# Performance work log

Measured on AMD Instinct MI355X. Metric: run time of the kernel, lower is better.

Reference implementation:

```python
import jax, jax.numpy as jnp
import numpy as np

N = 50000   # nodes
E = 640000  # edges
G = 128     # graphs in batch
H = 128     # hidden_channels
F_NODE, F_EDGE, F_LIG, F_POC = 64, 16, 200, 100
N_STACK = 3  # num_layers - 1


def setup_inputs() -> dict:
    key = jax.random.key(0)
    ks = jax.random.split(key, 24)
    r = lambda i, shape, s=0.05: jax.random.normal(ks[i], shape, dtype=jnp.float32) * s
    z = lambda shape: jnp.zeros(shape, jnp.float32)
    return {
        "x": jax.random.normal(ks[0], (N, F_NODE), dtype=jnp.float32),
        "edge_index": jax.random.randint(ks[1], (2, E), 0, N),
        "edge_attr": jax.random.normal(ks[2], (E, F_EDGE), dtype=jnp.float32),
        "batch": jnp.sort(jax.random.randint(ks[3], (N,), 0, G)),
        "ligand_features": jax.random.normal(ks[4], (G, F_LIG), dtype=jnp.float32),
        "pocket_features": jax.random.normal(ks[5], (G, F_POC), dtype=jnp.float32),
        # conv1 (in != out -> lin_self is a Linear)
        "W1_msg": r(6, (F_NODE, H)), "b1_msg": z((H,)),
        "W1_edge": r(7, (F_EDGE, H)), "b1_edge": z((H,)),
        "W1_self": r(8, (F_NODE, H)), "b1_self": z((H,)),
        # stacked convs (in == out -> lin_self is Identity)
        "Wk_msg": r(9, (N_STACK, H, H)), "bk_msg": z((N_STACK, H)),
        "Wk_edge": r(10, (N_STACK, F_EDGE, H)), "bk_edge": z((N_STACK, H)),
        # global feature / fusion / output heads
        "Wl": r(11, (F_LIG, H)), "bl": z((H,)),
        "Wp": r(12, (F_POC, H)), "bp": z((H,)),
        "Wf": r(13, (3 * H, H)), "bf": z((H,)),
        "Wo": r(14, (H, 1)), "bo": z((1,)),
        "return_embeddings": 0,
    }


def _general_conv(x, edge_index, edge_attr, W_msg, b_msg, W_edge, b_edge, self_out):
    # PyG GeneralConv: msg = lin_msg(x_src) + lin_edge(edge_attr), sum-aggregated at dst,
    # then + lin_self(x) (Identity skip when passed self_out = x).
    src, dst = edge_index[0], edge_index[1]
    edge_term = edge_attr @ W_edge + b_edge            # [E, H] (per-edge, layer-specific)
    msg = x[src] @ W_msg + b_msg + edge_term           # [E, H] gather + GEMM
    agg = jax.ops.segment_sum(msg, dst, num_segments=x.shape[0])  # scatter-add
    return agg + self_out


def reference(x, edge_index, edge_attr, batch, ligand_features, pocket_features,
              W1_msg, b1_msg, W1_edge, b1_edge, W1_self, b1_self,
              Wk_msg, bk_msg, Wk_edge, bk_edge,
              Wl, bl, Wp, bp, Wf, bf, Wo, bo, return_embeddings):
    # conv1 with linear self-connection
    h = _general_conv(x, edge_index, edge_attr, W1_msg, b1_msg, W1_edge, b1_edge,
                      x @ W1_self + b1_self)
    h = jax.nn.relu(h)
    # stacked convs with identity self-connection
    for i in range(N_STACK):
        h = _general_conv(h, edge_index, edge_attr, Wk_msg[i], bk_msg[i],
                          Wk_edge[i], bk_edge[i], h)
        h = jax.nn.relu(h)
    # global mean pool over graphs
    sums = jax.ops.segment_sum(h, batch, num_segments=G)
    counts = jax.ops.segment_sum(jnp.ones((h.shape[0],), h.dtype), batch, num_segments=G)
    pooled = sums / jnp.maximum(counts, 1.0)[:, None]
    # global feature fusion
    lig = ligand_features @ Wl + bl
    poc = pocket_features @ Wp + bp
    fused = jnp.concatenate([pooled, lig, poc], axis=1) @ Wf + bf
    # dropout is a no-op in eval mode
    if not return_embeddings:
        fused = fused @ Wo + bo
    return fused
```

## Files before the change

### kernel.cpp

```cpp
#include <hip/hip_runtime.h>
#include <cstdint>

#define NN 50000
#define NE 640000
#define NG 128
#define HD 128
#define FN 64
#define FE 16
#define FL 200
#define FPOC 100
#define NSTACK 3

typedef unsigned short ushort_t;
typedef short short8 __attribute__((ext_vector_type(8)));
typedef float f32x4 __attribute__((ext_vector_type(4)));

__device__ __forceinline__ ushort_t f2bf(float f) {
    unsigned u = __float_as_uint(f);
    unsigned r = (u + 0x7fffu + ((u >> 16) & 1u)) >> 16;
    return (ushort_t)r;
}
__device__ __forceinline__ float bf2f(ushort_t u) {
    return __uint_as_float(((unsigned)u) << 16);
}


__global__ void count_kernel(const int* __restrict__ ei, int* __restrict__ cnt) {
    int e = blockIdx.x * 256 + threadIdx.x;
    if (e < NE) atomicAdd(&cnt[ei[NE + e]], 1);
}

__global__ void bsum_kernel(const int* __restrict__ cnt, int* __restrict__ bsum) {
    __shared__ int s[256];
    int t = threadIdx.x;
    int i = blockIdx.x * 256 + t;
    int v = (i < NN) ? cnt[i] : 0;
    s[t] = v;
    __syncthreads();
    for (int off = 128; off > 0; off >>= 1) {
        if (t < off) s[t] += s[t + off];
        __syncthreads();
    }
    if (t == 0) bsum[blockIdx.x] = s[0];
}

__global__ void bscan_kernel(const int* __restrict__ bsum, int* __restrict__ bpre, int nb) {
    __shared__ int s[256];
    int t = threadIdx.x;
    int v = (t < nb) ? bsum[t] : 0;
    s[t] = v;
    __syncthreads();
    for (int off = 1; off < 256; off <<= 1) {
        int w = (t >= off) ? s[t - off] : 0;
        __syncthreads();
        s[t] += w;
        __syncthreads();
    }
    if (t < nb) bpre[t] = s[t] - v;
}

__global__ void rowptr_kernel(const int* __restrict__ cnt, const int* __restrict__ bpre,
                              int* __restrict__ row_ptr) {
    __shared__ int s[256];
    int t = threadIdx.x;
    int i = blockIdx.x * 256 + t;
    int v = (i < NN) ? cnt[i] : 0;
    s[t] = v;
    __syncthreads();
    for (int off = 1; off < 256; off <<= 1) {
        int w = (t >= off) ? s[t - off] : 0;
        __syncthreads();
        s[t] += w;
        __syncthreads();
    }
    if (i < NN) row_ptr[i] = s[t] - v + bpre[blockIdx.x];
    if (i == 0) row_ptr[NN] = NE;
}

__global__ void fill_kernel(const int* __restrict__ ei, const int* __restrict__ row_ptr,
                            int* __restrict__ cnt, int2* __restrict__ csr) {
    int e = blockIdx.x * 256 + threadIdx.x;
    if (e < NE) {
        int s = ei[e];
        int d = ei[NE + e];
        int old = atomicSub(&cnt[d], 1);
        csr[row_ptr[d] + old - 1] = make_int2(s, e);
    }
}

__global__ __launch_bounds__(256) void sege_kernel(
    const int* __restrict__ row_ptr, const int2* __restrict__ csr,
    const float* __restrict__ ea, ushort_t* __restrict__ segaug) {
    int node = blockIdx.x * 4 + (threadIdx.x >> 6);
    if (node >= NN) return;
    int lane = threadIdx.x & 63;
    int G = lane >> 2, q4 = (lane & 3) * 4;
    int beg = row_ptr[node], end = row_ptr[node + 1];
    float4 a = make_float4(0.f, 0.f, 0.f, 0.f);
    for (int j = beg + G; j < end; j += 16) {
        int e = csr[j].y;
        float4 v = *(const float4*)(ea + (size_t)e * FE + q4);
        a.x += v.x; a.y += v.y; a.z += v.z; a.w += v.w;
    }
    for (int m = 4; m <= 32; m <<= 1) {
        a.x += __shfl_xor(a.x, m);
        a.y += __shfl_xor(a.y, m);
        a.z += __shfl_xor(a.z, m);
        a.w += __shfl_xor(a.w, m);
    }
    if (lane < 4) {
        ushort_t o[4] = {f2bf(a.x), f2bf(a.y), f2bf(a.z), f2bf(a.w)};
        *(uint2*)(segaug + (size_t)node * 32 + lane * 4) = *(uint2*)o;
    } else if (lane < 8) {
        ushort_t o[4] = {0, 0, 0, 0};
        if (lane == 4) { o[0] = f2bf((float)(end - beg)); o[1] = f2bf(1.f); }
        *(uint2*)(segaug + (size_t)node * 32 + lane * 4) = *(uint2*)o;
    }
}


__global__ void repack_kernel(const float* __restrict__ W1_msg,
                              const float* __restrict__ W1_self,
                              const float* __restrict__ W1_edge,
                              const float* __restrict__ b1_msg,
                              const float* __restrict__ b1_edge,
                              const float* __restrict__ b1_self,
                              const float* __restrict__ Wk_msg,
                              const float* __restrict__ Wk_edge,
                              const float* __restrict__ bk_msg,
                              const float* __restrict__ bk_edge,
                              ushort_t* __restrict__ pack) {
    int mid = blockIdx.y;
    const float *W = nullptr, *bm = nullptr, *be = nullptr, *bc = nullptr;
    int K;
    size_t doff;
    bool aug = false;
    if (mid == 0)      { W = W1_msg;  K = 64;  doff = 0; }
    else if (mid == 1) { W = W1_self; K = 64;  doff = 8192; }
    else if (mid == 2) { W = W1_edge; bm = b1_msg; be = b1_edge; bc = b1_self;
                         K = 32; doff = 16384; aug = true; }
    else if (mid <= 5) { int i = mid - 3; W = Wk_msg + (size_t)i * HD * HD;
                         K = 128; doff = 20480 + (size_t)i * 16384; }
    else               { int i = mid - 6; W = Wk_edge + (size_t)i * FE * HD;
                         bm = bk_msg + i * HD; be = bk_edge + i * HD;
                         K = 32; doff = 69632 + (size_t)i * 4096; aug = true; }
    int KS = K / 32;
    int t = blockIdx.x * 256 + threadIdx.x;
    if (t >= 8 * KS * 64) return;
    int lane = t & 63;
    int nk = t >> 6;
    int ks = nk % KS, nt = nk / KS;
    int n = nt * 16 + (lane & 15);
    int kb = ks * 32 + (lane >> 4) * 8;
    ushort_t o[8];
#pragma unroll
    for (int j = 0; j < 8; ++j) {
        int k = kb + j;
        float v;
        if (!aug)         v = W[(size_t)k * HD + n];
        else if (k < 16)  v = W[(size_t)k * HD + n];
        else if (k == 16) v = bm[n] + be[n];
        else if (k == 17) v = bc ? bc[n] : 0.f;
        else              v = 0.f;
        o[j] = f2bf(v);
    }
    *(uint4*)(pack + doff + (size_t)t * 8) = *(uint4*)o;
}


__global__ __launch_bounds__(256) void gemm_mfma_conv1(const float* __restrict__ A,
                                                       const ushort_t* __restrict__ segaug,
                                                       const ushort_t* __restrict__ pack,
                                                       ushort_t* __restrict__ Cm,
                                                       ushort_t* __restrict__ Cs, int n) {
    constexpr int STR = 72, SSTR = 40;
    __shared__ __align__(16) ushort_t As[64 * STR];
    __shared__ __align__(16) ushort_t Ss[64 * SSTR];
    int tid = threadIdx.x;
    int row0 = blockIdx.x * 64;
#pragma unroll
    for (int p = 0; p < 2; ++p) {
        int c = p * 256 + tid;
        int r = c >> 3, col = (c & 7) * 8;
        int gr = row0 + r;
        float4 f0 = make_float4(0.f, 0.f, 0.f, 0.f), f1 = f0;
        if (gr < n) {
            f0 = *(const float4*)(A + (size_t)gr * FN + col);
            f1 = *(const float4*)(A + (size_t)gr * FN + col + 4);
        }
        ushort_t o[8] = {f2bf(f0.x), f2bf(f0.y), f2bf(f0.z), f2bf(f0.w),
                         f2bf(f1.x), f2bf(f1.y), f2bf(f1.z), f2bf(f1.w)};
        *(uint4*)(&As[r * STR + col]) = *(uint4*)o;
    }
    {
        int c = tid;
        int r = c >> 2, col = (c & 3) * 8;
        int gr = row0 + r;
        uint4 v = make_uint4(0u, 0u, 0u, 0u);
        if (gr < n) v = *(const uint4*)(segaug + (size_t)gr * 32 + col);
        *(uint4*)(&Ss[r * SSTR + col]) = v;
    }
    __syncthreads();
    int lane = tid & 63, wave = tid >> 6;
    int m = lane & 15, quad = lane >> 4;
    f32x4 acc[16];
#pragma unroll
    for (int i = 0; i < 16; ++i) acc[i] = (f32x4)(0.f);
    const short8* Bmsg = (const short8*)pack;
    const short8* Bself = (const short8*)(pack + 8192);
    const short8* Beaug = (const short8*)(pack + 16384);
#pragma unroll
    for (int ks = 0; ks < 2; ++ks) {
        short8 a = *(const short8*)(&As[(wave * 16 + m) * STR + ks * 32 + quad * 8]);
#pragma unroll
        for (int nt = 0; nt < 8; ++nt) {
            acc[nt] = __builtin_amdgcn_mfma_f32_16x16x32_bf16(
                a, Bmsg[(nt * 2 + ks) * 64 + lane], acc[nt], 0, 0, 0);
            acc[8 + nt] = __builtin_amdgcn_mfma_f32_16x16x32_bf16(
                a, Bself[(nt * 2 + ks) * 64 + lane], acc[8 + nt], 0, 0, 0);
        }
    }
    {
        short8 sa = *(const short8*)(&Ss[(wave * 16 + m) * SSTR + quad * 8]);
#pragma unroll
        for (int nt = 0; nt < 8; ++nt)
            acc[8 + nt] = __builtin_amdgcn_mfma_f32_16x16x32_bf16(
                sa, Beaug[nt * 64 + lane], acc[8 + nt], 0, 0, 0);
    }
#pragma unroll
    for (int nt = 0; nt < 8; ++nt) {
        int col = nt * 16 + m;
#pragma unroll
        for (int r = 0; r < 4; ++r) {
            int grow = row0 + wave * 16 + quad * 4 + r;
            if (grow < n) {
                Cm[(size_t)grow * HD + col] = f2bf(acc[nt][r]);
                Cs[(size_t)grow * HD + col] = f2bf(acc[8 + nt][r]);
            }
        }
    }
}


__device__ __forceinline__ void accum8(float* a, uint4 v) {
    a[0] += __uint_as_float(v.x << 16);
    a[1] += __uint_as_float(v.x & 0xffff0000u);
    a[2] += __uint_as_float(v.y << 16);
    a[3] += __uint_as_float(v.y & 0xffff0000u);
    a[4] += __uint_as_float(v.z << 16);
    a[5] += __uint_as_float(v.z & 0xffff0000u);
    a[6] += __uint_as_float(v.w << 16);
    a[7] += __uint_as_float(v.w & 0xffff0000u);
}

__global__ __launch_bounds__(256, 6) void fused_agg_gemm(
    const int* __restrict__ row_ptr, const int2* __restrict__ csr,
    const ushort_t* __restrict__ msg_in, const ushort_t* __restrict__ S_in,
    const ushort_t* __restrict__ segaug, const ushort_t* __restrict__ Bm,
    const ushort_t* __restrict__ Be, ushort_t* __restrict__ msg_out,
    ushort_t* __restrict__ S_out) {
    constexpr int STR = 136, SSTR = 40;
    __shared__ __align__(16) ushort_t Hs[16 * STR];
    __shared__ __align__(16) ushort_t Ss[16 * SSTR];
    int tid = threadIdx.x;
    int node0 = blockIdx.x * 16;
    if (tid < 64) {
        int r = tid >> 2, col = (tid & 3) * 8;
        *(uint4*)(&Ss[r * SSTR + col]) =
            *(const uint4*)(segaug + (size_t)(node0 + r) * 32 + col);
    }
    int nl = tid >> 4;
    int node = node0 + nl;
    int c8 = (tid & 15) * 8;
    int beg = row_ptr[node], end = row_ptr[node + 1];
    float a0[8] = {0.f, 0.f, 0.f, 0.f, 0.f, 0.f, 0.f, 0.f};
    float a1[8] = {0.f, 0.f, 0.f, 0.f, 0.f, 0.f, 0.f, 0.f};
    int j = beg;
    for (; j + 3 < end; j += 4) {
        int u0 = csr[j].x, u1 = csr[j + 1].x, u2 = csr[j + 2].x, u3 = csr[j + 3].x;
        uint4 v0 = *(const uint4*)(msg_in + (size_t)u0 * HD + c8);
        uint4 v1 = *(const uint4*)(msg_in + (size_t)u1 * HD + c8);
        uint4 v2 = *(const uint4*)(msg_in + (size_t)u2 * HD + c8);
        uint4 v3 = *(const uint4*)(msg_in + (size_t)u3 * HD + c8);
        accum8(a0, v0);
        accum8(a1, v1);
        accum8(a0, v2);
        accum8(a1, v3);
    }
    for (; j < end; ++j) {
        uint4 v = *(const uint4*)(msg_in + (size_t)csr[j].x * HD + c8);
        accum8(a0, v);
    }
    accum8(a0, *(const uint4*)(S_in + (size_t)node * HD + c8));
    {
        ushort_t h8[8];
#pragma unroll
        for (int i = 0; i < 8; ++i) h8[i] = f2bf(fmaxf(a0[i] + a1[i], 0.f));
        *(uint4*)(&Hs[nl * STR + c8]) = *(uint4*)h8;
    }
    __syncthreads();
    int lane = tid & 63, wave = tid >> 6;
    int m = lane & 15, quad = lane >> 4;
    f32x4 acc[2], accE[2];
#pragma unroll
    for (int t = 0; t < 2; ++t) { acc[t] = (f32x4)(0.f); accE[t] = (f32x4)(0.f); }
    const short8* Bmv = (const short8*)Bm;
    const short8* Bev = (const short8*)Be;
#pragma unroll
    for (int ks = 0; ks < 4; ++ks) {
        short8 a = *(const short8*)(&Hs[m * STR + ks * 32 + quad * 8]);
#pragma unroll
        for (int t = 0; t < 2; ++t) {
            int nt = wave * 2 + t;
            acc[t] = __builtin_amdgcn_mfma_f32_16x16x32_bf16(
                a, Bmv[(nt * 4 + ks) * 64 + lane], acc[t], 0, 0, 0);
        }
    }
    {
        short8 sa = *(const short8*)(&Ss[m * SSTR + quad * 8]);
#pragma unroll
        for (int t = 0; t < 2; ++t) {
            int nt = wave * 2 + t;
            accE[t] = __builtin_amdgcn_mfma_f32_16x16x32_bf16(
                sa, Bev[nt * 64 + lane], accE[t], 0, 0, 0);
        }
    }
#pragma unroll
    for (int t = 0; t < 2; ++t) {
        int col = (wave * 2 + t) * 16 + m;
#pragma unroll
        for (int r = 0; r < 4; ++r) {
            int rl = quad * 4 + r;
            size_t gidx = (size_t)(node0 + rl) * HD + col;
            msg_out[gidx] = f2bf(acc[t][r]);
            S_out[gidx] = f2bf(accE[t][r] + bf2f(Hs[rl * STR + col]));
        }
    }
}


__global__ __launch_bounds__(256, 6) void agg_pool_kernel(
    const int* __restrict__ row_ptr, const int2* __restrict__ csr,
    const ushort_t* __restrict__ xm, const ushort_t* __restrict__ selfb,
    const int* __restrict__ batch, float* __restrict__ pooled) {
    __shared__ float hloc[16][HD];
    int tid = threadIdx.x;
    int node0 = blockIdx.x * 16;
    int nl = tid >> 4;
    int node = node0 + nl;
    int c8 = (tid & 15) * 8;
    int beg = row_ptr[node], end = row_ptr[node + 1];
    float a0[8] = {0.f, 0.f, 0.f, 0.f, 0.f, 0.f, 0.f, 0.f};
    float a1[8] = {0.f, 0.f, 0.f, 0.f, 0.f, 0.f, 0.f, 0.f};
    int j = beg;
    for (; j + 3 < end; j += 4) {
        int u0 = csr[j].x, u1 = csr[j + 1].x, u2 = csr[j + 2].x, u3 = csr[j + 3].x;
        uint4 v0 = *(const uint4*)(xm + (size_t)u0 * HD + c8);
        uint4 v1 = *(const uint4*)(xm + (size_t)u1 * HD + c8);
        uint4 v2 = *(const uint4*)(xm + (size_t)u2 * HD + c8);
        uint4 v3 = *(const uint4*)(xm + (size_t)u3 * HD + c8);
        accum8(a0, v0);
        accum8(a1, v1);
        accum8(a0, v2);
        accum8(a1, v3);
    }
    for (; j < end; ++j) {
        uint4 v = *(const uint4*)(xm + (size_t)csr[j].x * HD + c8);
        accum8(a0, v);
    }
    accum8(a0, *(const uint4*)(selfb + (size_t)node * HD + c8));
#pragma unroll
    for (int i = 0; i < 8; ++i) hloc[nl][c8 + i] = fmaxf(a0[i] + a1[i], 0.f);
    __syncthreads();
    if (tid < HD) {
        int f = tid;
        float run = 0.f;
        int gprev = batch[node0];
        for (int r = 0; r < 16; ++r) {
            int g = batch[node0 + r];
            if (g != gprev) {
                atomicAdd(&pooled[gprev * HD + f], run);
                run = 0.f;
                gprev = g;
            }
            run += hloc[r][f];
        }
        atomicAdd(&pooled[gprev * HD + f], run);
    }
}


__global__ void head_kernel(const float* __restrict__ pooled, const int* __restrict__ batch,
                            const float* __restrict__ lf, const float* __restrict__ pfe,
                            const float* __restrict__ Wl, const float* __restrict__ bl,
                            const float* __restrict__ Wp, const float* __restrict__ bp,
                            const float* __restrict__ Wf, const float* __restrict__ bfv,
                            const float* __restrict__ Wo, const float* __restrict__ bo,
                            float* __restrict__ out) {
    __shared__ float cat[3 * HD];
    __shared__ float red[HD];
    int g = blockIdx.x, j = threadIdx.x;
    int lo = 0, hi = NN;
    while (lo < hi) { int m = (lo + hi) >> 1; if (batch[m] < g) lo = m + 1; else hi = m; }
    int s0 = lo;
    lo = s0; hi = NN;
    while (lo < hi) { int m = (lo + hi) >> 1; if (batch[m] < g + 1) lo = m + 1; else hi = m; }
    float cntf = (float)(lo - s0);
    cat[j] = pooled[(size_t)g * HD + j] / fmaxf(cntf, 1.f);
    float s = bl[j];
    for (int k = 0; k < FL; ++k) s += lf[g * FL + k] * Wl[k * HD + j];
    cat[HD + j] = s;
    s = bp[j];
    for (int k = 0; k < FPOC; ++k) s += pfe[g * FPOC + k] * Wp[k * HD + j];
    cat[2 * HD + j] = s;
    __syncthreads();
    float fj = bfv[j];
    for (int k = 0; k < 3 * HD; ++k) fj += cat[k] * Wf[k * HD + j];
    red[j] = fj * Wo[j];
    __syncthreads();
    for (int off = 64; off > 0; off >>= 1) {
        if (j < off) red[j] += red[j + off];
        __syncthreads();
    }
    if (j == 0) out[g] = red[0] + bo[0];
}


extern "C" void kernel_launch(void* const* d_in, const int* in_sizes, int n_in,
                              void* d_out, int out_size, void* d_ws, size_t ws_size,
                              hipStream_t stream) {
    const float* x       = (const float*)d_in[0];
    const int*   ei      = (const int*)d_in[1];
    const float* ea      = (const float*)d_in[2];
    const int*   batch   = (const int*)d_in[3];
    const float* lf      = (const float*)d_in[4];
    const float* pfe     = (const float*)d_in[5];
    const float* W1_msg  = (const float*)d_in[6];
    const float* b1_msg  = (const float*)d_in[7];
    const float* W1_edge = (const float*)d_in[8];
    const float* b1_edge = (const float*)d_in[9];
    const float* W1_self = (const float*)d_in[10];
    const float* b1_self = (const float*)d_in[11];
    const float* Wk_msg  = (const float*)d_in[12];
    const float* bk_msg  = (const float*)d_in[13];
    const float* Wk_edge = (const float*)d_in[14];
    const float* bk_edge = (const float*)d_in[15];
    const float* Wl      = (const float*)d_in[16];
    const float* bl      = (const float*)d_in[17];
    const float* Wp      = (const float*)d_in[18];
    const float* bp      = (const float*)d_in[19];
    const float* Wf      = (const float*)d_in[20];
    const float* bfv     = (const float*)d_in[21];
    const float* Wo      = (const float*)d_in[22];
    const float* bo      = (const float*)d_in[23];

    char* wsp = (char*)d_ws;
    size_t off = 0;
    auto carve = [&](size_t bytes) -> void* {
        char* p = wsp + off;
        off += (bytes + 255) & ~(size_t)255;
        return (void*)p;
    };
    int*      cnt     = (int*)carve((size_t)NN * 4);
    float*    pooled  = (float*)carve((size_t)NG * HD * 4);
    int*      row_ptr = (int*)carve((size_t)(NN + 1) * 4);
    int2*     csr     = (int2*)carve((size_t)NE * 8);
    ushort_t* segaug  = (ushort_t*)carve((size_t)NN * 32 * 2);
    ushort_t* pack    = (ushort_t*)carve((size_t)81920 * 2);
    ushort_t* bufC    = (ushort_t*)carve((size_t)NN * HD * 2);
    ushort_t* bufD    = (ushort_t*)carve((size_t)NN * HD * 2);
    ushort_t* bufS    = (ushort_t*)carve((size_t)NN * HD * 2);
    ushort_t* bufT    = (ushort_t*)carve((size_t)NN * HD * 2);
    int*      bsum    = (int*)carve((size_t)256 * 4);
    int*      bpre    = (int*)carve((size_t)256 * 4);

    const int NBLK = (NN + 255) / 256;

    size_t clr = (size_t)((char*)(pooled + NG * HD) - (char*)cnt);
    hipMemsetAsync(cnt, 0, clr, stream);

    count_kernel<<<(NE + 255) / 256, 256, 0, stream>>>(ei, cnt);
    bsum_kernel<<<NBLK, 256, 0, stream>>>(cnt, bsum);
    bscan_kernel<<<1, 256, 0, stream>>>(bsum, bpre, NBLK);
    rowptr_kernel<<<NBLK, 256, 0, stream>>>(cnt, bpre, row_ptr);
    fill_kernel<<<(NE + 255) / 256, 256, 0, stream>>>(ei, row_ptr, cnt, csr);
    sege_kernel<<<(NN + 3) / 4, 256, 0, stream>>>(row_ptr, csr, ea, segaug);
    repack_kernel<<<dim3(8, 9), 256, 0, stream>>>(W1_msg, W1_self, W1_edge, b1_msg,
                                                  b1_edge, b1_self, Wk_msg, Wk_edge,
                                                  bk_msg, bk_edge, pack);

    gemm_mfma_conv1<<<dim3((NN + 63) / 64), 256, 0, stream>>>(x, segaug, pack, bufC,
                                                              bufS, NN);
    fused_agg_gemm<<<NN / 16, 256, 0, stream>>>(row_ptr, csr, bufC, bufS, segaug,
                                                pack + 20480, pack + 69632, bufD, bufT);
    fused_agg_gemm<<<NN / 16, 256, 0, stream>>>(row_ptr, csr, bufD, bufT, segaug,
                                                pack + 20480 + 16384, pack + 69632 + 4096,
                                                bufC, bufS);
    fused_agg_gemm<<<NN / 16, 256, 0, stream>>>(row_ptr, csr, bufC, bufS, segaug,
                                                pack + 20480 + 32768, pack + 69632 + 8192,
                                                bufD, bufT);
    agg_pool_kernel<<<NN / 16, 256, 0, stream>>>(row_ptr, csr, bufD, bufT, batch, pooled);

    head_kernel<<<NG, HD, 0, stream>>>(pooled, batch, lf, pfe, Wl, bl, Wp, bp, Wf, bfv,
                                       Wo, bo, (float*)d_out);
}
```

Baseline: 388.3 us.

## Build CSR with atomic block allocation and stage neighbor indices in LDS

The three-kernel prefix scan is replaced by a single alloc kernel. Each 256-node block takes its base offset with one atomicAdd, and fill uses per-node cursors, so row_ptr becomes row_beg plus cnt and two launches go away. The aggregation kernels copy each 16-node tile's source indices into shared memory, unroll the gather loop to 8 loads in flight, and prefetch the self row, aiming for more memory-level parallelism in the irregular gather. Segment order across blocks becomes nondeterministic, and the extra LDS plus the launch-bounds change from 6 to 5 may reduce occupancy.

```diff
diff --git a/kernel.cpp b/kernel.cpp
--- a/kernel.cpp
+++ b/kernel.cpp
@@ -10,6 +10,7 @@
 #define FL 200
 #define FPOC 100
 #define NSTACK 3
+#define EDGE_CAP 512
 
 typedef unsigned short ushort_t;
 typedef short short8 __attribute__((ext_vector_type(8)));
@@ -30,24 +31,13 @@
     if (e < NE) atomicAdd(&cnt[ei[NE + e]], 1);
 }
 
-__global__ void bsum_kernel(const int* __restrict__ cnt, int* __restrict__ bsum) {
+__global__ void alloc_kernel(const int* __restrict__ cnt, int* __restrict__ row_beg,
+                             int* __restrict__ cur, int* __restrict__ gtot) {
     __shared__ int s[256];
+    __shared__ int base;
     int t = threadIdx.x;
     int i = blockIdx.x * 256 + t;
     int v = (i < NN) ? cnt[i] : 0;
-    s[t] = v;
-    __syncthreads();
-    for (int off = 128; off > 0; off >>= 1) {
-        if (t < off) s[t] += s[t + off];
-        __syncthreads();
-    }
-    if (t == 0) bsum[blockIdx.x] = s[0];
-}
-
-__global__ void bscan_kernel(const int* __restrict__ bsum, int* __restrict__ bpre, int nb) {
-    __shared__ int s[256];
-    int t = threadIdx.x;
-    int v = (t < nb) ? bsum[t] : 0;
     s[t] = v;
     __syncthreads();
     for (int off = 1; off < 256; off <<= 1) {
@@ -56,46 +46,37 @@
         s[t] += w;
         __syncthreads();
     }
-    if (t < nb) bpre[t] = s[t] - v;
-}
-
-__global__ void rowptr_kernel(const int* __restrict__ cnt, const int* __restrict__ bpre,
-                              int* __restrict__ row_ptr) {
-    __shared__ int s[256];
-    int t = threadIdx.x;
-    int i = blockIdx.x * 256 + t;
-    int v = (i < NN) ? cnt[i] : 0;
-    s[t] = v;
-    __syncthreads();
-    for (int off = 1; off < 256; off <<= 1) {
-        int w = (t >= off) ? s[t - off] : 0;
-        __syncthreads();
-        s[t] += w;
-        __syncthreads();
-    }
-    if (i < NN) row_ptr[i] = s[t] - v + bpre[blockIdx.x];
-    if (i == 0) row_ptr[NN] = NE;
-}
-
-__global__ void fill_kernel(const int* __restrict__ ei, const int* __restrict__ row_ptr,
-                            int* __restrict__ cnt, int2* __restrict__ csr) {
+    if (t == 255) base = atomicAdd(gtot, s[255]);
+    __syncthreads();
+    if (i < NN) {
+        int b = base + s[t] - v;
+        row_beg[i] = b;
+        cur[i] = b;
+    }
+}
+
+__global__ void fill_kernel(const int* __restrict__ ei, int* __restrict__ cur,
+                            int2* __restrict__ csr) {
     int e = blockIdx.x * 256 + threadIdx.x;
     if (e < NE) {
         int s = ei[e];
         int d = ei[NE + e];
-        int old = atomicSub(&cnt[d], 1);
-        csr[row_ptr[d] + old - 1] = make_int2(s, e);
+        int pos = atomicAdd(&cur[d], 1);
+        csr[pos] = make_int2(s, e);
     }
 }
 
 __global__ __launch_bounds__(256) void sege_kernel(
-    const int* __restrict__ row_ptr, const int2* __restrict__ csr,
-    const float* __restrict__ ea, ushort_t* __restrict__ segaug) {
+    const int* __restrict__ row_beg, const int* __restrict__ cnt,
+    const int2* __restrict__ csr, const float* __restrict__ ea,
+    ushort_t* __restrict__ segaug) {
     int node = blockIdx.x * 4 + (threadIdx.x >> 6);
     if (node >= NN) return;
     int lane = threadIdx.x & 63;
     int G = lane >> 2, q4 = (lane & 3) * 4;
-    int beg = row_ptr[node], end = row_ptr[node + 1];
+    int beg = row_beg[node];
+    int dg = cnt[node];
+    int end = beg + dg;
     float4 a = make_float4(0.f, 0.f, 0.f, 0.f);
     for (int j = beg + G; j < end; j += 16) {
         int e = csr[j].y;
@@ -113,7 +94,7 @@
         *(uint2*)(segaug + (size_t)node * 32 + lane * 4) = *(uint2*)o;
     } else if (lane < 8) {
         ushort_t o[4] = {0, 0, 0, 0};
-        if (lane == 4) { o[0] = f2bf((float)(end - beg)); o[1] = f2bf(1.f); }
+        if (lane == 4) { o[0] = f2bf((float)dg); o[1] = f2bf(1.f); }
         *(uint2*)(segaug + (size_t)node * 32 + lane * 4) = *(uint2*)o;
     }
 }
@@ -253,15 +234,47 @@
     a[7] += __uint_as_float(v.w & 0xffff0000u);
 }
 
-__global__ __launch_bounds__(256, 6) void fused_agg_gemm(
-    const int* __restrict__ row_ptr, const int2* __restrict__ csr,
-    const ushort_t* __restrict__ msg_in, const ushort_t* __restrict__ S_in,
-    const ushort_t* __restrict__ segaug, const ushort_t* __restrict__ Bm,
-    const ushort_t* __restrict__ Be, ushort_t* __restrict__ msg_out,
-    ushort_t* __restrict__ S_out) {
+#define GET_LDS(jj) (ce[lb + (jj)])
+#define GET_GBL(jj) (csr[(size_t)(beg + (jj))].x)
+
+#define AGG_BODY(GET)                                                        \
+    {                                                                        \
+        int j = 0;                                                           \
+        for (; j + 7 < d; j += 8) {                                          \
+            int u[8];                                                        \
+            _Pragma("unroll") for (int t = 0; t < 8; ++t) u[t] = GET(j + t); \
+            uint4 v[8];                                                      \
+            _Pragma("unroll") for (int t = 0; t < 8; ++t)                    \
+                v[t] = *(const uint4*)(msg_in + (size_t)u[t] * HD + c8);     \
+            _Pragma("unroll") for (int t = 0; t < 8; ++t)                    \
+                accum8((t & 1) ? a1 : a0, v[t]);                             \
+        }                                                                    \
+        if (j + 3 < d) {                                                     \
+            int u[4];                                                        \
+            _Pragma("unroll") for (int t = 0; t < 4; ++t) u[t] = GET(j + t); \
+            uint4 v[4];                                                      \
+            _Pragma("unroll") for (int t = 0; t < 4; ++t)                    \
+                v[t] = *(const uint4*)(msg_in + (size_t)u[t] * HD + c8);     \
+            _Pragma("unroll") for (int t = 0; t < 4; ++t)                    \
+                accum8((t & 1) ? a1 : a0, v[t]);                             \
+            j += 4;                                                          \
+        }                                                                    \
+        for (; j < d; ++j) {                                                 \
+            uint4 v = *(const uint4*)(msg_in + (size_t)GET(j) * HD + c8);    \
+            accum8(a0, v);                                                   \
+        }                                                                    \
+    }
+
+__global__ __launch_bounds__(256, 5) void fused_agg_gemm(
+    const int* __restrict__ row_beg, const int* __restrict__ cnt,
+    const int2* __restrict__ csr, const ushort_t* __restrict__ msg_in,
+    const ushort_t* __restrict__ S_in, const ushort_t* __restrict__ segaug,
+    const ushort_t* __restrict__ Bm, const ushort_t* __restrict__ Be,
+    ushort_t* __restrict__ msg_out, ushort_t* __restrict__ S_out) {
     constexpr int STR = 136, SSTR = 40;
     __shared__ __align__(16) ushort_t Hs[16 * STR];
     __shared__ __align__(16) ushort_t Ss[16 * SSTR];
+    __shared__ int ce[EDGE_CAP];
     int tid = threadIdx.x;
     int node0 = blockIdx.x * 16;
     if (tid < 64) {
@@ -269,29 +282,26 @@
         *(uint4*)(&Ss[r * SSTR + col]) =
             *(const uint4*)(segaug + (size_t)(node0 + r) * 32 + col);
     }
+    int b0 = row_beg[node0];
+    int nE = row_beg[node0 + 15] + cnt[node0 + 15] - b0;
+    int stg = nE < EDGE_CAP ? nE : EDGE_CAP;
+    for (int i = tid; i < stg; i += 256) ce[i] = csr[b0 + i].x;
     int nl = tid >> 4;
     int node = node0 + nl;
     int c8 = (tid & 15) * 8;
-    int beg = row_ptr[node], end = row_ptr[node + 1];
+    int beg = row_beg[node];
+    int d = cnt[node];
+    int lb = beg - b0;
+    uint4 sv = *(const uint4*)(S_in + (size_t)node * HD + c8);
+    __syncthreads();
     float a0[8] = {0.f, 0.f, 0.f, 0.f, 0.f, 0.f, 0.f, 0.f};
     float a1[8] = {0.f, 0.f, 0.f, 0.f, 0.f, 0.f, 0.f, 0.f};
-    int j = beg;
-    for (; j + 3 < end; j += 4) {
-        int u0 = csr[j].x, u1 = csr[j + 1].x, u2 = csr[j + 2].x, u3 = csr[j + 3].x;
-        uint4 v0 = *(const uint4*)(msg_in + (size_t)u0 * HD + c8);
-        uint4 v1 = *(const uint4*)(msg_in + (size_t)u1 * HD + c8);
-        uint4 v2 = *(const uint4*)(msg_in + (size_t)u2 * HD + c8);
-        uint4 v3 = *(const uint4*)(msg_in + (size_t)u3 * HD + c8);
-        accum8(a0, v0);
-        accum8(a1, v1);
-        accum8(a0, v2);
-        accum8(a1, v3);
-    }
-    for (; j < end; ++j) {
-        uint4 v = *(const uint4*)(msg_in + (size_t)csr[j].x * HD + c8);
-        accum8(a0, v);
-    }
-    accum8(a0, *(const uint4*)(S_in + (size_t)node * HD + c8));
+    if (lb + d <= EDGE_CAP) {
+        AGG_BODY(GET_LDS)
+    } else {
+        AGG_BODY(GET_GBL)
+    }
+    accum8(a0, sv);
     {
         ushort_t h8[8];
 #pragma unroll
@@ -339,36 +349,36 @@
 }
 
 
-__global__ __launch_bounds__(256, 6) void agg_pool_kernel(
-    const int* __restrict__ row_ptr, const int2* __restrict__ csr,
-    const ushort_t* __restrict__ xm, const ushort_t* __restrict__ selfb,
-    const int* __restrict__ batch, float* __restrict__ pooled) {
+__global__ __launch_bounds__(256, 5) void agg_pool_kernel(
+    const int* __restrict__ row_beg, const int* __restrict__ cnt,
+    const int2* __restrict__ csr, const ushort_t* __restrict__ xm,
+    const ushort_t* __restrict__ selfb, const int* __restrict__ batch,
+    float* __restrict__ pooled) {
     __shared__ float hloc[16][HD];
+    __shared__ int ce[EDGE_CAP];
     int tid = threadIdx.x;
     int node0 = blockIdx.x * 16;
+    int b0 = row_beg[node0];
+    int nE = row_beg[node0 + 15] + cnt[node0 + 15] - b0;
+    int stg = nE < EDGE_CAP ? nE : EDGE_CAP;
+    for (int i = tid; i < stg; i += 256) ce[i] = csr[b0 + i].x;
     int nl = tid >> 4;
     int node = node0 + nl;
     int c8 = (tid & 15) * 8;
-    int beg = row_ptr[node], end = row_ptr[node + 1];
+    int beg = row_beg[node];
+    int d = cnt[node];
+    int lb = beg - b0;
+    const ushort_t* msg_in = xm;
+    uint4 sv = *(const uint4*)(selfb + (size_t)node * HD + c8);
+    __syncthreads();
     float a0[8] = {0.f, 0.f, 0.f, 0.f, 0.f, 0.f, 0.f, 0.f};
     float a1[8] = {0.f, 0.f, 0.f, 0.f, 0.f, 0.f, 0.f, 0.f};
-    int j = beg;
-    for (; j + 3 < end; j += 4) {
-        int u0 = csr[j].x, u1 = csr[j + 1].x, u2 = csr[j + 2].x, u3 = csr[j + 3].x;
-        uint4 v0 = *(const uint4*)(xm + (size_t)u0 * HD + c8);
-        uint4 v1 = *(const uint4*)(xm + (size_t)u1 * HD + c8);
-        uint4 v2 = *(const uint4*)(xm + (size_t)u2 * HD + c8);
-        uint4 v3 = *(const uint4*)(xm + (size_t)u3 * HD + c8);
-        accum8(a0, v0);
-        accum8(a1, v1);
-        accum8(a0, v2);
-        accum8(a1, v3);
-    }
-    for (; j < end; ++j) {
-        uint4 v = *(const uint4*)(xm + (size_t)csr[j].x * HD + c8);
-        accum8(a0, v);
-    }
-    accum8(a0, *(const uint4*)(selfb + (size_t)node * HD + c8));
+    if (lb + d <= EDGE_CAP) {
+        AGG_BODY(GET_LDS)
+    } else {
+        AGG_BODY(GET_GBL)
+    }
+    accum8(a0, sv);
 #pragma unroll
     for (int i = 0; i < 8; ++i) hloc[nl][c8 + i] = fmaxf(a0[i] + a1[i], 0.f);
     __syncthreads();
@@ -462,8 +472,10 @@
         return (void*)p;
     };
     int*      cnt     = (int*)carve((size_t)NN * 4);
+    int*      misc    = (int*)carve(256);
     float*    pooled  = (float*)carve((size_t)NG * HD * 4);
-    int*      row_ptr = (int*)carve((size_t)(NN + 1) * 4);
+    int*      row_beg = (int*)carve((size_t)NN * 4);
+    int*      cur     = (int*)carve((size_t)NN * 4);
     int2*     csr     = (int2*)carve((size_t)NE * 8);
     ushort_t* segaug  = (ushort_t*)carve((size_t)NN * 32 * 2);
     ushort_t* pack    = (ushort_t*)carve((size_t)81920 * 2);
@@ -471,8 +483,6 @@
     ushort_t* bufD    = (ushort_t*)carve((size_t)NN * HD * 2);
     ushort_t* bufS    = (ushort_t*)carve((size_t)NN * HD * 2);
     ushort_t* bufT    = (ushort_t*)carve((size_t)NN * HD * 2);
-    int*      bsum    = (int*)carve((size_t)256 * 4);
-    int*      bpre    = (int*)carve((size_t)256 * 4);
 
     const int NBLK = (NN + 255) / 256;
 
@@ -480,26 +490,25 @@
     hipMemsetAsync(cnt, 0, clr, stream);
 
     count_kernel<<<(NE + 255) / 256, 256, 0, stream>>>(ei, cnt);
-    bsum_kernel<<<NBLK, 256, 0, stream>>>(cnt, bsum);
-    bscan_kernel<<<1, 256, 0, stream>>>(bsum, bpre, NBLK);
-    rowptr_kernel<<<NBLK, 256, 0, stream>>>(cnt, bpre, row_ptr);
-    fill_kernel<<<(NE + 255) / 256, 256, 0, stream>>>(ei, row_ptr, cnt, csr);
-    sege_kernel<<<(NN + 3) / 4, 256, 0, stream>>>(row_ptr, csr, ea, segaug);
+    alloc_kernel<<<NBLK, 256, 0, stream>>>(cnt, row_beg, cur, misc);
+    fill_kernel<<<(NE + 255) / 256, 256, 0, stream>>>(ei, cur, csr);
+    sege_kernel<<<(NN + 3) / 4, 256, 0, stream>>>(row_beg, cnt, csr, ea, segaug);
     repack_kernel<<<dim3(8, 9), 256, 0, stream>>>(W1_msg, W1_self, W1_edge, b1_msg,
                                                   b1_edge, b1_self, Wk_msg, Wk_edge,
                                                   bk_msg, bk_edge, pack);
 
     gemm_mfma_conv1<<<dim3((NN + 63) / 64), 256, 0, stream>>>(x, segaug, pack, bufC,
                                                               bufS, NN);
-    fused_agg_gemm<<<NN / 16, 256, 0, stream>>>(row_ptr, csr, bufC, bufS, segaug,
+    fused_agg_gemm<<<NN / 16, 256, 0, stream>>>(row_beg, cnt, csr, bufC, bufS, segaug,
                                                 pack + 20480, pack + 69632, bufD, bufT);
-    fused_agg_gemm<<<NN / 16, 256, 0, stream>>>(row_ptr, csr, bufD, bufT, segaug,
+    fused_agg_gemm<<<NN / 16, 256, 0, stream>>>(row_beg, cnt, csr, bufD, bufT, segaug,
                                                 pack + 20480 + 16384, pack + 69632 + 4096,
                                                 bufC, bufS);
-    fused_agg_gemm<<<NN / 16, 256, 0, stream>>>(row_ptr, csr, bufC, bufS, segaug,
+    fused_agg_gemm<<<NN / 16, 256, 0, stream>>>(row_beg, cnt, csr, bufC, bufS, segaug,
                                                 pack + 20480 + 32768, pack + 69632 + 8192,
                                                 bufD, bufT);
-    agg_pool_kernel<<<NN / 16, 256, 0, stream>>>(row_ptr, csr, bufD, bufT, batch, pooled);
+    agg_pool_kernel<<<NN / 16, 256, 0, stream>>>(row_beg, cnt, csr, bufD, bufT, batch,
+                                                 pooled);
 
     head_kernel<<<NG, HD, 0, stream>>>(pooled, batch, lf, pfe, Wl, bl, Wp, bp, Wf, bfv,
                                        Wo, bo, (float*)d_out);
```

Result: slower. 397.3 us (+2.3%).

## Build CSR via two-level bucket sort with shared-memory atomics

Applied to the files above, without the earlier changes.

Replaces the per-node global-atomic count, three-kernel scan and global-atomic fill with a bucketed counting sort. Edges are first binned into 196 buckets of 256 destination nodes using shared-memory histograms and a staging buffer. A per-bucket kernel then computes node offsets and places edges with shared-memory atomics. Downstream kernels switch from row_ptr to row_beg plus a count. This cuts global atomic contention and kernel launches, at the cost of an extra staging array and a second pass over the edges.

```diff
diff --git a/kernel.cpp b/kernel.cpp
--- a/kernel.cpp
+++ b/kernel.cpp
@@ -10,6 +10,7 @@
 #define FL 200
 #define FPOC 100
 #define NSTACK 3
+#define NBUK 196
 
 typedef unsigned short ushort_t;
 typedef short short8 __attribute__((ext_vector_type(8)));
@@ -25,29 +26,26 @@
 }
 
 
-__global__ void count_kernel(const int* __restrict__ ei, int* __restrict__ cnt) {
-    int e = blockIdx.x * 256 + threadIdx.x;
-    if (e < NE) atomicAdd(&cnt[ei[NE + e]], 1);
-}
-
-__global__ void bsum_kernel(const int* __restrict__ cnt, int* __restrict__ bsum) {
+__global__ void hist_kernel(const int* __restrict__ ei, int* __restrict__ bucket_cnt) {
+    __shared__ int l[NBUK];
+    int t = threadIdx.x;
+    if (t < NBUK) l[t] = 0;
+    __syncthreads();
+    int base = blockIdx.x * 2048;
+#pragma unroll
+    for (int i = 0; i < 8; ++i) {
+        int e = base + i * 256 + t;
+        if (e < NE) atomicAdd(&l[ei[NE + e] >> 8], 1);
+    }
+    __syncthreads();
+    if (t < NBUK && l[t]) atomicAdd(&bucket_cnt[t], l[t]);
+}
+
+__global__ void scan_kernel(const int* __restrict__ bucket_cnt,
+                            int* __restrict__ bucket_base, int* __restrict__ bucket_cur) {
     __shared__ int s[256];
     int t = threadIdx.x;
-    int i = blockIdx.x * 256 + t;
-    int v = (i < NN) ? cnt[i] : 0;
-    s[t] = v;
-    __syncthreads();
-    for (int off = 128; off > 0; off >>= 1) {
-        if (t < off) s[t] += s[t + off];
-        __syncthreads();
-    }
-    if (t == 0) bsum[blockIdx.x] = s[0];
-}
-
-__global__ void bscan_kernel(const int* __restrict__ bsum, int* __restrict__ bpre, int nb) {
-    __shared__ int s[256];
-    int t = threadIdx.x;
-    int v = (t < nb) ? bsum[t] : 0;
+    int v = (t < NBUK) ? bucket_cnt[t] : 0;
     s[t] = v;
     __syncthreads();
     for (int off = 1; off < 256; off <<= 1) {
@@ -56,46 +54,97 @@
         s[t] += w;
         __syncthreads();
     }
-    if (t < nb) bpre[t] = s[t] - v;
-}
-
-__global__ void rowptr_kernel(const int* __restrict__ cnt, const int* __restrict__ bpre,
-                              int* __restrict__ row_ptr) {
-    __shared__ int s[256];
+    if (t < NBUK) {
+        int b = s[t] - v;
+        bucket_base[t] = b;
+        bucket_cur[t] = b;
+    }
+}
+
+__global__ __launch_bounds__(256) void scatter_bin(const int* __restrict__ ei,
+                                                   int* __restrict__ bucket_cur,
+                                                   int2* __restrict__ staging) {
+    __shared__ int lcnt[NBUK];
+    __shared__ int lrun[NBUK];
     int t = threadIdx.x;
-    int i = blockIdx.x * 256 + t;
-    int v = (i < NN) ? cnt[i] : 0;
-    s[t] = v;
+    if (t < NBUK) lcnt[t] = 0;
+    __syncthreads();
+    int base = blockIdx.x * 4096;
+#pragma unroll
+    for (int i = 0; i < 16; ++i) {
+        int e = base + i * 256 + t;
+        if (e < NE) atomicAdd(&lcnt[ei[NE + e] >> 8], 1);
+    }
+    __syncthreads();
+    if (t < NBUK) {
+        int c = lcnt[t];
+        lrun[t] = c ? atomicAdd(&bucket_cur[t], c) : 0;
+        lcnt[t] = 0;
+    }
+    __syncthreads();
+#pragma unroll
+    for (int i = 0; i < 16; ++i) {
+        int e = base + i * 256 + t;
+        if (e < NE) {
+            int s = ei[e];
+            int d = ei[NE + e];
+            int bk = d >> 8;
+            int off = atomicAdd(&lcnt[bk], 1);
+            staging[lrun[bk] + off] = make_int2(s, e | ((d & 255) << 20));
+        }
+    }
+}
+
+__global__ __launch_bounds__(256) void place_kernel(
+    const int* __restrict__ bucket_base, const int* __restrict__ bucket_cnt,
+    const int2* __restrict__ staging, int* __restrict__ row_beg,
+    int* __restrict__ cnt, int2* __restrict__ csr) {
+    __shared__ int hist[256];
+    __shared__ int curp[256];
+    int t = threadIdx.x;
+    int b = blockIdx.x;
+    int n0 = b << 8;
+    hist[t] = 0;
+    __syncthreads();
+    int ebase = bucket_base[b];
+    int ecnt = bucket_cnt[b];
+    for (int i = t; i < ecnt; i += 256) atomicAdd(&hist[staging[ebase + i].y >> 20], 1);
+    __syncthreads();
+    int v = hist[t];
     __syncthreads();
     for (int off = 1; off < 256; off <<= 1) {
-        int w = (t >= off) ? s[t - off] : 0;
+        int w = (t >= off) ? hist[t - off] : 0;
         __syncthreads();
-        s[t] += w;
+        hist[t] += w;
         __syncthreads();
     }
-    if (i < NN) row_ptr[i] = s[t] - v + bpre[blockIdx.x];
-    if (i == 0) row_ptr[NN] = NE;
-}
-
-__global__ void fill_kernel(const int* __restrict__ ei, const int* __restrict__ row_ptr,
-                            int* __restrict__ cnt, int2* __restrict__ csr) {
-    int e = blockIdx.x * 256 + threadIdx.x;
-    if (e < NE) {
-        int s = ei[e];
-        int d = ei[NE + e];
-        int old = atomicSub(&cnt[d], 1);
-        csr[row_ptr[d] + old - 1] = make_int2(s, e);
+    int rb = ebase + hist[t] - v;
+    if (n0 + t < NN) {
+        row_beg[n0 + t] = rb;
+        cnt[n0 + t] = v;
+    }
+    curp[t] = rb;
+    __syncthreads();
+    for (int i = t; i < ecnt; i += 256) {
+        int2 p = staging[ebase + i];
+        int dl = p.y >> 20;
+        int e = p.y & 0xFFFFF;
+        int pos = atomicAdd(&curp[dl], 1);
+        csr[pos] = make_int2(p.x, e);
     }
 }
 
 __global__ __launch_bounds__(256) void sege_kernel(
-    const int* __restrict__ row_ptr, const int2* __restrict__ csr,
-    const float* __restrict__ ea, ushort_t* __restrict__ segaug) {
+    const int* __restrict__ row_beg, const int* __restrict__ cnt,
+    const int2* __restrict__ csr, const float* __restrict__ ea,
+    ushort_t* __restrict__ segaug) {
     int node = blockIdx.x * 4 + (threadIdx.x >> 6);
     if (node >= NN) return;
     int lane = threadIdx.x & 63;
     int G = lane >> 2, q4 = (lane & 3) * 4;
-    int beg = row_ptr[node], end = row_ptr[node + 1];
+    int beg = row_beg[node];
+    int dg = cnt[node];
+    int end = beg + dg;
     float4 a = make_float4(0.f, 0.f, 0.f, 0.f);
     for (int j = beg + G; j < end; j += 16) {
         int e = csr[j].y;
@@ -113,7 +162,7 @@
         *(uint2*)(segaug + (size_t)node * 32 + lane * 4) = *(uint2*)o;
     } else if (lane < 8) {
         ushort_t o[4] = {0, 0, 0, 0};
-        if (lane == 4) { o[0] = f2bf((float)(end - beg)); o[1] = f2bf(1.f); }
+        if (lane == 4) { o[0] = f2bf((float)dg); o[1] = f2bf(1.f); }
         *(uint2*)(segaug + (size_t)node * 32 + lane * 4) = *(uint2*)o;
     }
 }
@@ -254,11 +303,11 @@
 }
 
 __global__ __launch_bounds__(256, 6) void fused_agg_gemm(
-    const int* __restrict__ row_ptr, const int2* __restrict__ csr,
-    const ushort_t* __restrict__ msg_in, const ushort_t* __restrict__ S_in,
-    const ushort_t* __restrict__ segaug, const ushort_t* __restrict__ Bm,
-    const ushort_t* __restrict__ Be, ushort_t* __restrict__ msg_out,
-    ushort_t* __restrict__ S_out) {
+    const int* __restrict__ row_beg, const int* __restrict__ cnt,
+    const int2* __restrict__ csr, const ushort_t* __restrict__ msg_in,
+    const ushort_t* __restrict__ S_in, const ushort_t* __restrict__ segaug,
+    const ushort_t* __restrict__ Bm, const ushort_t* __restrict__ Be,
+    ushort_t* __restrict__ msg_out, ushort_t* __restrict__ S_out) {
     constexpr int STR = 136, SSTR = 40;
     __shared__ __align__(16) ushort_t Hs[16 * STR];
     __shared__ __align__(16) ushort_t Ss[16 * SSTR];
@@ -272,7 +321,8 @@
     int nl = tid >> 4;
     int node = node0 + nl;
     int c8 = (tid & 15) * 8;
-    int beg = row_ptr[node], end = row_ptr[node + 1];
+    int beg = row_beg[node];
+    int end = beg + cnt[node];
     float a0[8] = {0.f, 0.f, 0.f, 0.f, 0.f, 0.f, 0.f, 0.f};
     float a1[8] = {0.f, 0.f, 0.f, 0.f, 0.f, 0.f, 0.f, 0.f};
     int j = beg;
@@ -340,16 +390,18 @@
 
 
 __global__ __launch_bounds__(256, 6) void agg_pool_kernel(
-    const int* __restrict__ row_ptr, const int2* __restrict__ csr,
-    const ushort_t* __restrict__ xm, const ushort_t* __restrict__ selfb,
-    const int* __restrict__ batch, float* __restrict__ pooled) {
+    const int* __restrict__ row_beg, const int* __restrict__ cnt,
+    const int2* __restrict__ csr, const ushort_t* __restrict__ xm,
+    const ushort_t* __restrict__ selfb, const int* __restrict__ batch,
+    float* __restrict__ pooled) {
     __shared__ float hloc[16][HD];
     int tid = threadIdx.x;
     int node0 = blockIdx.x * 16;
     int nl = tid >> 4;
     int node = node0 + nl;
     int c8 = (tid & 15) * 8;
-    int beg = row_ptr[node], end = row_ptr[node + 1];
+    int beg = row_beg[node];
+    int end = beg + cnt[node];
     float a0[8] = {0.f, 0.f, 0.f, 0.f, 0.f, 0.f, 0.f, 0.f};
     float a1[8] = {0.f, 0.f, 0.f, 0.f, 0.f, 0.f, 0.f, 0.f};
     int j = beg;
@@ -461,45 +513,46 @@
         off += (bytes + 255) & ~(size_t)255;
         return (void*)p;
     };
-    int*      cnt     = (int*)carve((size_t)NN * 4);
-    float*    pooled  = (float*)carve((size_t)NG * HD * 4);
-    int*      row_ptr = (int*)carve((size_t)(NN + 1) * 4);
-    int2*     csr     = (int2*)carve((size_t)NE * 8);
-    ushort_t* segaug  = (ushort_t*)carve((size_t)NN * 32 * 2);
-    ushort_t* pack    = (ushort_t*)carve((size_t)81920 * 2);
-    ushort_t* bufC    = (ushort_t*)carve((size_t)NN * HD * 2);
-    ushort_t* bufD    = (ushort_t*)carve((size_t)NN * HD * 2);
-    ushort_t* bufS    = (ushort_t*)carve((size_t)NN * HD * 2);
-    ushort_t* bufT    = (ushort_t*)carve((size_t)NN * HD * 2);
-    int*      bsum    = (int*)carve((size_t)256 * 4);
-    int*      bpre    = (int*)carve((size_t)256 * 4);
-
-    const int NBLK = (NN + 255) / 256;
-
-    size_t clr = (size_t)((char*)(pooled + NG * HD) - (char*)cnt);
-    hipMemsetAsync(cnt, 0, clr, stream);
-
-    count_kernel<<<(NE + 255) / 256, 256, 0, stream>>>(ei, cnt);
-    bsum_kernel<<<NBLK, 256, 0, stream>>>(cnt, bsum);
-    bscan_kernel<<<1, 256, 0, stream>>>(bsum, bpre, NBLK);
-    rowptr_kernel<<<NBLK, 256, 0, stream>>>(cnt, bpre, row_ptr);
-    fill_kernel<<<(NE + 255) / 256, 256, 0, stream>>>(ei, row_ptr, cnt, csr);
-    sege_kernel<<<(NN + 3) / 4, 256, 0, stream>>>(row_ptr, csr, ea, segaug);
+    int*      bucket_cnt  = (int*)carve((size_t)NBUK * 4);
+    float*    pooled      = (float*)carve((size_t)NG * HD * 4);
+    int*      bucket_base = (int*)carve((size_t)NBUK * 4);
+    int*      bucket_cur  = (int*)carve((size_t)NBUK * 4);
+    int*      row_beg     = (int*)carve((size_t)NN * 4);
+    int*      cnt         = (int*)carve((size_t)NN * 4);
+    int2*     staging     = (int2*)carve((size_t)NE * 8);
+    int2*     csr         = (int2*)carve((size_t)NE * 8);
+    ushort_t* segaug      = (ushort_t*)carve((size_t)NN * 32 * 2);
+    ushort_t* pack        = (ushort_t*)carve((size_t)81920 * 2);
+    ushort_t* bufC        = (ushort_t*)carve((size_t)NN * HD * 2);
+    ushort_t* bufD        = (ushort_t*)carve((size_t)NN * HD * 2);
+    ushort_t* bufS        = (ushort_t*)carve((size_t)NN * HD * 2);
+    ushort_t* bufT        = (ushort_t*)carve((size_t)NN * HD * 2);
+
+    size_t clr = (size_t)((char*)(pooled + NG * HD) - (char*)bucket_cnt);
+    hipMemsetAsync(bucket_cnt, 0, clr, stream);
+
+    hist_kernel<<<(NE + 2047) / 2048, 256, 0, stream>>>(ei, bucket_cnt);
+    scan_kernel<<<1, 256, 0, stream>>>(bucket_cnt, bucket_base, bucket_cur);
+    scatter_bin<<<(NE + 4095) / 4096, 256, 0, stream>>>(ei, bucket_cur, staging);
+    place_kernel<<<NBUK, 256, 0, stream>>>(bucket_base, bucket_cnt, staging, row_beg,
+                                           cnt, csr);
+    sege_kernel<<<(NN + 3) / 4, 256, 0, stream>>>(row_beg, cnt, csr, ea, segaug);
     repack_kernel<<<dim3(8, 9), 256, 0, stream>>>(W1_msg, W1_self, W1_edge, b1_msg,
                                                   b1_edge, b1_self, Wk_msg, Wk_edge,
                                                   bk_msg, bk_edge, pack);
 
     gemm_mfma_conv1<<<dim3((NN + 63) / 64), 256, 0, stream>>>(x, segaug, pack, bufC,
                                                               bufS, NN);
-    fused_agg_gemm<<<NN / 16, 256, 0, stream>>>(row_ptr, csr, bufC, bufS, segaug,
+    fused_agg_gemm<<<NN / 16, 256, 0, stream>>>(row_beg, cnt, csr, bufC, bufS, segaug,
                                                 pack + 20480, pack + 69632, bufD, bufT);
-    fused_agg_gemm<<<NN / 16, 256, 0, stream>>>(row_ptr, csr, bufD, bufT, segaug,
+    fused_agg_gemm<<<NN / 16, 256, 0, stream>>>(row_beg, cnt, csr, bufD, bufT, segaug,
                                                 pack + 20480 + 16384, pack + 69632 + 4096,
                                                 bufC, bufS);
-    fused_agg_gemm<<<NN / 16, 256, 0, stream>>>(row_ptr, csr, bufC, bufS, segaug,
+    fused_agg_gemm<<<NN / 16, 256, 0, stream>>>(row_beg, cnt, csr, bufC, bufS, segaug,
                                                 pack + 20480 + 32768, pack + 69632 + 8192,
                                                 bufD, bufT);
-    agg_pool_kernel<<<NN / 16, 256, 0, stream>>>(row_ptr, csr, bufD, bufT, batch, pooled);
+    agg_pool_kernel<<<NN / 16, 256, 0, stream>>>(row_beg, cnt, csr, bufD, bufT, batch,
+                                                 pooled);
 
     head_kernel<<<NG, HD, 0, stream>>>(pooled, batch, lf, pfe, Wl, bl, Wp, bp, Wf, bfv,
                                        Wo, bo, (float*)d_out);
```

After: 356.8 us. 8.1% less time.
